# Performance work log

Hardware: AMD Instinct MI355X
Metric: run time of the kernel (lower is better)

Reference implementation:

```python
import jax, jax.numpy as jnp
import numpy as np

B, T, C, H = 2, 2048, 1024, 16
D = C // H  # head dim = 64
NEG_MIN = jnp.finfo(jnp.float32).min


def setup_inputs() -> dict:
    key = jax.random.key(0)
    ks = jax.random.split(key, 5)
    std = 0.02
    return {
        "x": jax.random.normal(ks[0], (B, T, C), dtype=jnp.float32),
        "Wq": std * jax.random.normal(ks[1], (C, C), dtype=jnp.float32),
        "bq": jnp.zeros((C,), dtype=jnp.float32),
        "Wk": std * jax.random.normal(ks[2], (C, C), dtype=jnp.float32),
        "bk": jnp.zeros((C,), dtype=jnp.float32),
        "Wv": std * jax.random.normal(ks[3], (C, C), dtype=jnp.float32),
        "bv": jnp.zeros((C,), dtype=jnp.float32),
        "Wo": (std / np.sqrt(24.0)) * jax.random.normal(ks[4], (C, C), dtype=jnp.float32),
        "bo": jnp.zeros((C,), dtype=jnp.float32),
    }


def reference(x, Wq, bq, Wk, bk, Wv, bv, Wo, bo):
    # QKV projections -> (B, H, T, D)
    def proj(W, b):
        return (x @ W + b).reshape(B, T, H, D).transpose(0, 2, 1, 3)

    q = proj(Wq, bq)
    k = proj(Wk, bk)
    v = proj(Wv, bv)

    # full scores (B, H, T, T), causal mask, softmax
    attn = jnp.einsum("bhqd,bhkd->bhqk", q, k) / jnp.sqrt(jnp.float32(D))
    mask = jnp.tril(jnp.ones((T, T), dtype=bool))[None, None]
    attn = jnp.where(mask, attn, NEG_MIN)
    scores = jax.nn.softmax(attn, axis=-1)

    out = jnp.einsum("bhqk,bhkd->bhqd", scores, v)
    out = out.transpose(0, 2, 1, 3).reshape(B, T, C)
    return out @ Wo + bo
```

## Files before the change

### kernel.cpp

```cpp
#include <hip/hip_runtime.h>
#include <stdint.h>
#include <stddef.h>


#define B_SZ 2
#define T_SZ 2048
#define C_SZ 1024
#define H_SZ 16
#define D_SZ 64
#define M_SZ (B_SZ * T_SZ)
#define BHTD (B_SZ * H_SZ * T_SZ * D_SZ)
#define CC (C_SZ * C_SZ)
#define SM_SHIFT 12.0f

typedef __attribute__((ext_vector_type(8))) __bf16 bf16x8;
typedef __attribute__((ext_vector_type(4))) float f32x4;
typedef __attribute__((ext_vector_type(16))) float f32x16;

__device__ __forceinline__ unsigned short f2bf(float f) {
    union { float f; unsigned u; } v; v.f = f;
    v.u += 0x7fffu + ((v.u >> 16) & 1u);
    return (unsigned short)(v.u >> 16);
}

__device__ __forceinline__ unsigned pkbf(float lo, float hi_) {
    union { unsigned u; __bf16 h[2]; } r;
    r.h[0] = (__bf16)lo; r.h[1] = (__bf16)hi_;
    return r.u;
}

__device__ __forceinline__ float fexp2(float x) {
    float r;
    asm volatile("v_exp_f32 %0, %1\n\ts_nop 0" : "=v"(r) : "v"(x));
    return r;
}

__device__ __forceinline__ void load_lds16(const unsigned short* g, unsigned short* l) {
    __builtin_amdgcn_global_load_lds(
        (const __attribute__((address_space(1))) void*)g,
        (__attribute__((address_space(3))) void*)l, 16, 0, 0);
}


__global__ void cvt_x_kernel(const float4* __restrict__ in, ushort4* __restrict__ out, int n4) {
    int stride = gridDim.x * blockDim.x;
    for (int i = blockIdx.x * blockDim.x + threadIdx.x; i < n4; i += stride) {
        float4 v = in[i];
        ushort4 o;
        o.x = f2bf(v.x); o.y = f2bf(v.y); o.z = f2bf(v.z); o.w = f2bf(v.w);
        out[i] = o;
    }
}

__global__ __launch_bounds__(256) void transpose_cvt_kernel(
    const float* __restrict__ W0, const float* __restrict__ W1,
    const float* __restrict__ W2, const float* __restrict__ W3,
    unsigned short* __restrict__ T0, unsigned short* __restrict__ T1,
    unsigned short* __restrict__ T2, unsigned short* __restrict__ T3)
{
    __shared__ float tile[32][33];
    const float* W; unsigned short* Wt;
    switch (blockIdx.z) {
        case 0: W = W0; Wt = T0; break;
        case 1: W = W1; Wt = T1; break;
        case 2: W = W2; Wt = T2; break;
        default: W = W3; Wt = T3; break;
    }
    const int tx = threadIdx.x, ty = threadIdx.y;
    const int n0 = blockIdx.x * 32, k0 = blockIdx.y * 32;
    #pragma unroll
    for (int i = 0; i < 4; i++)
        tile[ty + i * 8][tx] = W[(size_t)(k0 + ty + i * 8) * C_SZ + n0 + tx];
    __syncthreads();
    #pragma unroll
    for (int i = 0; i < 4; i++)
        Wt[(size_t)(n0 + ty + i * 8) * C_SZ + k0 + tx] = f2bf(tile[tx][ty + i * 8]);
}

__global__ __launch_bounds__(256) void vt_kernel(
    const unsigned short* __restrict__ V, unsigned short* __restrict__ Vt)
{
    __shared__ unsigned short tile[32][33];
    const int bh = blockIdx.z;
    const int t0 = blockIdx.x * 32, d0 = blockIdx.y * 32;
    const unsigned short* src = V + (size_t)bh * T_SZ * D_SZ;
    unsigned short* dst = Vt + (size_t)bh * T_SZ * D_SZ;
    const int tx = threadIdx.x, ty = threadIdx.y;
    #pragma unroll
    for (int i = 0; i < 4; i++)
        tile[ty + i * 8][tx] = src[(size_t)(t0 + ty + i * 8) * D_SZ + d0 + tx];
    __syncthreads();
    #pragma unroll
    for (int i = 0; i < 4; i++)
        dst[(size_t)(d0 + ty + i * 8) * T_SZ + t0 + tx] = tile[tx][ty + i * 8];
}


__device__ __forceinline__ void gemm_tile_core(
    const unsigned short* __restrict__ A,
    const unsigned short* __restrict__ Bt,
    unsigned short* As, unsigned short* Bs,
    int m0, int n0, f32x4 acc[4][4])
{
    const int tid = threadIdx.x;
    const int lane = tid & 63;
    const int w = tid >> 6;
    const int l15 = lane & 15, lg = lane >> 4;
    const int wr = (w >> 1) * 64, wc = (w & 1) * 64;

    const unsigned short* Ag0 = A + (size_t)(m0 + (tid >> 2)) * C_SZ + (tid & 3) * 8;
    const unsigned short* Ag1 = Ag0 + (size_t)64 * C_SZ;
    const unsigned short* Bg0 = Bt + (size_t)(n0 + (tid >> 2)) * C_SZ + (tid & 3) * 8;
    const unsigned short* Bg1 = Bg0 + (size_t)64 * C_SZ;
    unsigned short* As0 = As + w * 512;
    unsigned short* As1 = As + 2048 + w * 512;
    unsigned short* Bs0 = Bs + w * 512;
    unsigned short* Bs1 = Bs + 2048 + w * 512;

    for (int k0 = 0; k0 < C_SZ; k0 += 32) {
        load_lds16(Ag0 + k0, As0);
        load_lds16(Ag1 + k0, As1);
        load_lds16(Bg0 + k0, Bs0);
        load_lds16(Bg1 + k0, Bs1);
        __syncthreads();
        bf16x8 af[4], bfv[4];
        const bf16x8* Ap = (const bf16x8*)As;
        const bf16x8* Bp = (const bf16x8*)Bs;
        #pragma unroll
        for (int m = 0; m < 4; m++) af[m] = Ap[(wr + m * 16 + l15) * 4 + lg];
        #pragma unroll
        for (int n = 0; n < 4; n++) bfv[n] = Bp[(wc + n * 16 + l15) * 4 + lg];
        #pragma unroll
        for (int m = 0; m < 4; m++)
            #pragma unroll
            for (int n = 0; n < 4; n++)
                acc[m][n] = __builtin_amdgcn_mfma_f32_16x16x32_bf16(af[m], bfv[n], acc[m][n], 0, 0, 0);
        __syncthreads();
    }
}

__global__ __launch_bounds__(256) void gemm_qkv_kernel(
    const unsigned short* __restrict__ A,
    const unsigned short* __restrict__ WtBase,
    const float* __restrict__ bq, const float* __restrict__ bk, const float* __restrict__ bv,
    unsigned short* __restrict__ QKV, unsigned short* __restrict__ Vtmp)
{
    __shared__ unsigned short As[4096], Bs[4096];
    const int z = blockIdx.x >> 3;
    const unsigned short* Bt = WtBase + (size_t)z * CC;
    const float* bias = (z == 0) ? bq : (z == 1) ? bk : bv;
    const float scale = (z == 0) ? 0.18033688011112042f : 1.0f;
    unsigned short* Out = (z == 2) ? Vtmp : QKV + (size_t)z * BHTD;

    f32x4 acc[4][4];
    f32x4 zero4 = {0.f, 0.f, 0.f, 0.f};
    #pragma unroll
    for (int m = 0; m < 4; m++)
        #pragma unroll
        for (int n = 0; n < 4; n++) acc[m][n] = zero4;

    const int m0 = blockIdx.y * 128, n0 = (blockIdx.x & 7) * 128;
    gemm_tile_core(A, Bt, As, Bs, m0, n0, acc);

    const int lane = threadIdx.x & 63;
    const int w = threadIdx.x >> 6;
    const int l15 = lane & 15, lg = lane >> 4;
    const int wr = (w >> 1) * 64, wc = (w & 1) * 64;
    #pragma unroll
    for (int n = 0; n < 4; n++) {
        const int col = n0 + wc + n * 16 + l15;
        const float bias_v = bias[col];
        const int h = col >> 6, d = col & 63;
        #pragma unroll
        for (int m = 0; m < 4; m++) {
            #pragma unroll
            for (int j = 0; j < 4; j++) {
                const int row = m0 + wr + m * 16 + lg * 4 + j;
                const int b = row >> 11, t = row & (T_SZ - 1);
                Out[(((size_t)(b * H_SZ + h)) * T_SZ + t) * D_SZ + d] =
                    f2bf((acc[m][n][j] + bias_v) * scale);
            }
        }
    }
}

__global__ __launch_bounds__(256) void gemm_out_kernel(
    const unsigned short* __restrict__ A,
    const unsigned short* __restrict__ Bt,
    const float* __restrict__ bo,
    float* __restrict__ Out)
{
    __shared__ unsigned short As[2048], Bs[4096];
    const int tid = threadIdx.x;
    const int lane = tid & 63;
    const int w = tid >> 6;
    const int l15 = lane & 15, lg = lane >> 4;
    const int wc = w * 32;
    const int m0 = blockIdx.y * 64, n0 = blockIdx.x * 128;

    const unsigned short* Ag  = A + (size_t)(m0 + (tid >> 2)) * C_SZ + (tid & 3) * 8;
    const unsigned short* Bg0 = Bt + (size_t)(n0 + (tid >> 2)) * C_SZ + (tid & 3) * 8;
    const unsigned short* Bg1 = Bg0 + (size_t)64 * C_SZ;
    unsigned short* As0 = As + w * 512;
    unsigned short* Bs0 = Bs + w * 512;
    unsigned short* Bs1 = Bs + 2048 + w * 512;

    f32x4 acc[4][2];
    f32x4 zero4 = {0.f, 0.f, 0.f, 0.f};
    #pragma unroll
    for (int m = 0; m < 4; m++)
        #pragma unroll
        for (int n = 0; n < 2; n++) acc[m][n] = zero4;

    for (int k0 = 0; k0 < C_SZ; k0 += 32) {
        load_lds16(Ag + k0, As0);
        load_lds16(Bg0 + k0, Bs0);
        load_lds16(Bg1 + k0, Bs1);
        __syncthreads();
        bf16x8 af[4], bfv[2];
        const bf16x8* Ap = (const bf16x8*)As;
        const bf16x8* Bp = (const bf16x8*)Bs;
        #pragma unroll
        for (int m = 0; m < 4; m++) af[m] = Ap[(m * 16 + l15) * 4 + lg];
        #pragma unroll
        for (int n = 0; n < 2; n++) bfv[n] = Bp[(wc + n * 16 + l15) * 4 + lg];
        #pragma unroll
        for (int m = 0; m < 4; m++)
            #pragma unroll
            for (int n = 0; n < 2; n++)
                acc[m][n] = __builtin_amdgcn_mfma_f32_16x16x32_bf16(af[m], bfv[n], acc[m][n], 0, 0, 0);
        __syncthreads();
    }

    #pragma unroll
    for (int n = 0; n < 2; n++) {
        const int col = n0 + wc + n * 16 + l15;
        const float bias_v = bo[col];
        #pragma unroll
        for (int m = 0; m < 4; m++) {
            #pragma unroll
            for (int j = 0; j < 4; j++) {
                const int row = m0 + m * 16 + lg * 4 + j;
                Out[(size_t)row * C_SZ + col] = acc[m][n][j] + bias_v;
            }
        }
    }
}

__global__ __launch_bounds__(512) void attn_fwd_kernel(
    const unsigned short* __restrict__ Q,
    const unsigned short* __restrict__ K,
    const unsigned short* __restrict__ Vt,
    unsigned short* __restrict__ O)
{
    const int idx = blockIdx.x;
    const int qt = (idx < 256) ? (15 - (idx >> 5)) : ((idx - 256) >> 5);
    const int bh = idx & 31;
    const int w8 = threadIdx.x >> 6;
    const int grp = w8 >> 2;
    const int wg = w8 & 3;
    const int lane = threadIdx.x & 63;
    const int l31 = lane & 31, hi = lane >> 5;
    const int qw = qt * 128 + 32 * wg;

    const unsigned short* Qh = Q + (size_t)bh * T_SZ * D_SZ;
    const unsigned short* Kh = K + (size_t)bh * T_SZ * D_SZ;
    const unsigned short* Vh = Vt + (size_t)bh * T_SZ * D_SZ;

    __shared__ __align__(16) unsigned short smem[32768];

    const int c0 = wg * 64 + lane;
    const int row0 = c0 >> 3;
    const int sw0 = (c0 & 7) ^ (row0 & 7);
    const int koff0 = row0 * 64 + sw0 * 8;
    const int voff0 = row0 * T_SZ + sw0 * 8;
    const int ldsb0 = wg * 512;
    unsigned short* gbase = smem + grp * 16384;

    bf16x8 qf[4];
    #pragma unroll
    for (int j = 0; j < 4; j++)
        qf[j] = *(const bf16x8*)&Qh[(size_t)(qw + l31) * D_SZ + j * 16 + 8 * hi];

    f32x16 acc[2];
    #pragma unroll
    for (int r = 0; r < 16; r++) { acc[0][r] = 0.f; acc[1][r] = 0.f; }
    float lrun = 0.f;

    const int tlast = (qw + 31) >> 6;
    const int ntb = qt + 1;
    const int tg0 = grp * ntb;
    const int qrow = qw + l31;
    const int swl = l31 & 7;

    {
        const unsigned short* Kt = Kh + (size_t)tg0 * 64 * D_SZ;
        const unsigned short* Vtt = Vh + tg0 * 64;
        load_lds16(Kt + koff0, gbase + ldsb0);
        load_lds16(Kt + koff0 + 2048, gbase + 2048 + ldsb0);
        load_lds16(Vtt + voff0, gbase + 4096 + ldsb0);
        load_lds16(Vtt + voff0 + 32 * T_SZ, gbase + 6144 + ldsb0);
    }

    for (int tt = 0; tt < ntb; ++tt) {
        const int tg = tg0 + tt;
        if (tt + 1 < ntb) {
            unsigned short* Bd = gbase + ((tt + 1) & 1) * 8192;
            const unsigned short* Kt = Kh + (size_t)(tg + 1) * 64 * D_SZ;
            const unsigned short* Vtt = Vh + (tg + 1) * 64;
            load_lds16(Kt + koff0, Bd + ldsb0);
            load_lds16(Kt + koff0 + 2048, Bd + 2048 + ldsb0);
            load_lds16(Vtt + voff0, Bd + 4096 + ldsb0);
            load_lds16(Vtt + voff0 + 32 * T_SZ, Bd + 6144 + ldsb0);
            asm volatile("s_waitcnt vmcnt(4)" ::: "memory");
        } else {
            asm volatile("s_waitcnt vmcnt(0)" ::: "memory");
        }
        __builtin_amdgcn_s_barrier();

        if (tg <= tlast) {
            const unsigned short* Ks = gbase + (tt & 1) * 8192;
            const unsigned short* Vs = Ks + 4096;
            const int k0 = tg * 64;

            f32x16 s[2];
            __builtin_amdgcn_s_setprio(1);
            #pragma unroll
            for (int kb = 0; kb < 2; ++kb) {
                bf16x8 kf[4];
                #pragma unroll
                for (int j = 0; j < 4; ++j) {
                    const int ch = (j * 2 + hi) ^ swl;
                    kf[j] = *(const bf16x8*)&Ks[(kb * 32 + l31) * 64 + ch * 8];
                }
                f32x16 sc;
                #pragma unroll
                for (int r = 0; r < 16; r++) sc[r] = 0.f;
                #pragma unroll
                for (int j = 0; j < 4; ++j)
                    sc = __builtin_amdgcn_mfma_f32_32x32x16_bf16(kf[j], qf[j], sc, 0, 0, 0);
                s[kb] = sc;
            }
            __builtin_amdgcn_s_setprio(0);

            if (k0 + 63 > qw) {
                #pragma unroll
                for (int kb = 0; kb < 2; ++kb)
                    #pragma unroll
                    for (int r = 0; r < 16; ++r) {
                        const int kv = k0 + kb * 32 + (r & 3) + 8 * (r >> 2) + 4 * hi;
                        s[kb][r] = (kv > qrow) ? -3.0e38f : s[kb][r];
                    }
            }

            #pragma unroll
            for (int kb = 0; kb < 2; ++kb)
                #pragma unroll
                for (int r = 0; r < 16; r++) s[kb][r] = fexp2(s[kb][r] - SM_SHIFT);

            float ps0 = s[0][0] + s[1][0], ps1 = s[0][1] + s[1][1];
            float ps2 = s[0][2] + s[1][2], ps3 = s[0][3] + s[1][3];
            #pragma unroll
            for (int r = 4; r < 16; r += 4) {
                ps0 += s[0][r + 0] + s[1][r + 0];
                ps1 += s[0][r + 1] + s[1][r + 1];
                ps2 += s[0][r + 2] + s[1][r + 2];
                ps3 += s[0][r + 3] + s[1][r + 3];
            }
            float ps = (ps0 + ps1) + (ps2 + ps3);
            ps += __shfl_xor(ps, 32);
            lrun += ps;

            bf16x8 pf[2][2];
            #pragma unroll
            for (int kb = 0; kb < 2; ++kb) {
                #pragma unroll
                for (int ksl = 0; ksl < 2; ++ksl) {
                    unsigned a0 = pkbf(s[kb][8 * ksl + 0], s[kb][8 * ksl + 1]);
                    unsigned a1 = pkbf(s[kb][8 * ksl + 2], s[kb][8 * ksl + 3]);
                    unsigned b0 = pkbf(s[kb][8 * ksl + 4], s[kb][8 * ksl + 5]);
                    unsigned b1 = pkbf(s[kb][8 * ksl + 6], s[kb][8 * ksl + 7]);
                    asm volatile("v_permlane32_swap_b32 %0, %1" : "+v"(a0), "+v"(b0));
                    asm volatile("v_permlane32_swap_b32 %0, %1" : "+v"(a1), "+v"(b1));
                    union { unsigned u[4]; bf16x8 v; } fr;
                    fr.u[0] = a0; fr.u[1] = a1; fr.u[2] = b0; fr.u[3] = b1;
                    pf[kb][ksl] = fr.v;
                }
            }

            __builtin_amdgcn_s_setprio(1);
            #pragma unroll
            for (int dt = 0; dt < 2; ++dt)
                #pragma unroll
                for (int kb = 0; kb < 2; ++kb)
                    #pragma unroll
                    for (int ksl = 0; ksl < 2; ++ksl) {
                        const int ks = kb * 2 + ksl;
                        const int ch = (ks * 2 + hi) ^ swl;
                        const bf16x8 vf = *(const bf16x8*)&Vs[(dt * 32 + l31) * 64 + ch * 8];
                        acc[dt] = __builtin_amdgcn_mfma_f32_32x32x16_bf16(vf, pf[kb][ksl], acc[dt], 0, 0, 0);
                    }
            __builtin_amdgcn_s_setprio(0);
        }
        __builtin_amdgcn_s_barrier();
    }

    float* accf = (float*)smem;
    float* lsh = accf + 256 * 33;
    if (grp == 1) {
        const int li = wg * 64 + lane;
        #pragma unroll
        for (int r = 0; r < 16; r++) {
            accf[li * 33 + r] = acc[0][r];
            accf[li * 33 + 16 + r] = acc[1][r];
        }
        if (hi == 0) lsh[wg * 32 + l31] = lrun;
    }
    __builtin_amdgcn_s_barrier();
    if (grp == 0) {
        const int li = wg * 64 + lane;
        const float l1 = lsh[wg * 32 + l31];
        const float inv = 1.0f / (lrun + l1);
        #pragma unroll
        for (int r = 0; r < 16; r++) {
            acc[0][r] = (acc[0][r] + accf[li * 33 + r]) * inv;
            acc[1][r] = (acc[1][r] + accf[li * 33 + 16 + r]) * inv;
        }
    }
    __builtin_amdgcn_s_barrier();

    if (grp == 0) {
        unsigned short* ot = smem + wg * 2304;
        #pragma unroll
        for (int g = 0; g < 4; g++) {
            ushort4 wa, wb;
            wa.x = f2bf(acc[0][4 * g + 0]); wa.y = f2bf(acc[0][4 * g + 1]);
            wa.z = f2bf(acc[0][4 * g + 2]); wa.w = f2bf(acc[0][4 * g + 3]);
            wb.x = f2bf(acc[1][4 * g + 0]); wb.y = f2bf(acc[1][4 * g + 1]);
            wb.z = f2bf(acc[1][4 * g + 2]); wb.w = f2bf(acc[1][4 * g + 3]);
            *(ushort4*)&ot[l31 * 72 + 8 * g + 4 * hi] = wa;
            *(ushort4*)&ot[l31 * 72 + 32 + 8 * g + 4 * hi] = wb;
        }
        const int b = bh >> 4, h = bh & 15;
        #pragma unroll
        for (int pss = 0; pss < 4; pss++) {
            const int q = pss * 8 + (lane >> 3);
            const uint4 val = *(const uint4*)&ot[q * 72 + (lane & 7) * 8];
            *(uint4*)&O[((size_t)(b * T_SZ + qw + q)) * C_SZ + h * D_SZ + (lane & 7) * 8] = val;
        }
    }
}


extern "C" void kernel_launch(void* const* d_in, const int* in_sizes, int n_in,
                              void* d_out, int out_size, void* d_ws, size_t ws_size,
                              hipStream_t stream)
{
    const float* x  = (const float*)d_in[0];
    const float* Wq = (const float*)d_in[1];
    const float* bq = (const float*)d_in[2];
    const float* Wk = (const float*)d_in[3];
    const float* bk = (const float*)d_in[4];
    const float* Wv = (const float*)d_in[5];
    const float* bv = (const float*)d_in[6];
    const float* Wo = (const float*)d_in[7];
    const float* bo = (const float*)d_in[8];

    uint8_t* ws = (uint8_t*)d_ws;
    unsigned short* XB   = (unsigned short*)(ws);
    unsigned short* WT   = (unsigned short*)(ws + (8u  << 20));
    unsigned short* QKV  = (unsigned short*)(ws + (16u << 20));
    unsigned short* Vtmp = (unsigned short*)(ws + (40u << 20));

    cvt_x_kernel<<<2048, 256, 0, stream>>>((const float4*)x, (ushort4*)XB, M_SZ * C_SZ / 4);
    transpose_cvt_kernel<<<dim3(32, 32, 4), dim3(32, 8), 0, stream>>>(
        Wq, Wk, Wv, Wo, WT, WT + CC, WT + 2 * (size_t)CC, WT + 3 * (size_t)CC);
    gemm_qkv_kernel<<<dim3(24, 32), 256, 0, stream>>>(XB, WT, bq, bk, bv, QKV, Vtmp);
    vt_kernel<<<dim3(64, 2, 32), dim3(32, 8), 0, stream>>>(Vtmp, QKV + 2 * (size_t)BHTD);
    attn_fwd_kernel<<<512, 512, 0, stream>>>(
        QKV, QKV + BHTD, QKV + 2 * (size_t)BHTD, Vtmp);
    gemm_out_kernel<<<dim3(8, 64), 256, 0, stream>>>(Vtmp, WT + 3 * (size_t)CC, bo, (float*)d_out);
}
```

Baseline: 115.6 us.

## Halve attention tiles to 64-query blocks and 32-key tiles with 4-wave workgroups

Restructures the attention kernel so each workgroup handles 64 query rows with 4 waves (2 per key-split group) instead of 128 rows with 8 waves. K/V tiles shrink from 64 to 32 keys, the LDS swizzle for V changes to a 4-chunk pattern, and the grid doubles to 1024 blocks. The aim is finer causal granularity, less wasted masked work, more blocks for load balance, and lower LDS use per block for higher occupancy. In exchange it doubles the number of loop iterations and barriers per key range and halves K/V reuse per load.

```diff
diff --git a/kernel.cpp b/kernel.cpp
--- a/kernel.cpp
+++ b/kernel.cpp
@@ -247,35 +247,37 @@
     }
 }
 
-__global__ __launch_bounds__(512) void attn_fwd_kernel(
+__global__ __launch_bounds__(256) void attn_fwd_kernel(
     const unsigned short* __restrict__ Q,
     const unsigned short* __restrict__ K,
     const unsigned short* __restrict__ Vt,
     unsigned short* __restrict__ O)
 {
     const int idx = blockIdx.x;
-    const int qt = (idx < 256) ? (15 - (idx >> 5)) : ((idx - 256) >> 5);
+    const int qb = (idx < 512) ? (31 - (idx >> 5)) : ((idx - 512) >> 5);
     const int bh = idx & 31;
-    const int w8 = threadIdx.x >> 6;
-    const int grp = w8 >> 2;
-    const int wg = w8 & 3;
+    const int w4 = threadIdx.x >> 6;
+    const int grp = w4 >> 1;
+    const int wg = w4 & 1;
     const int lane = threadIdx.x & 63;
     const int l31 = lane & 31, hi = lane >> 5;
-    const int qw = qt * 128 + 32 * wg;
+    const int qw = qb * 64 + 32 * wg;
 
     const unsigned short* Qh = Q + (size_t)bh * T_SZ * D_SZ;
     const unsigned short* Kh = K + (size_t)bh * T_SZ * D_SZ;
     const unsigned short* Vh = Vt + (size_t)bh * T_SZ * D_SZ;
 
-    __shared__ __align__(16) unsigned short smem[32768];
+    __shared__ __align__(16) unsigned short smem[16384];
 
     const int c0 = wg * 64 + lane;
-    const int row0 = c0 >> 3;
-    const int sw0 = (c0 & 7) ^ (row0 & 7);
-    const int koff0 = row0 * 64 + sw0 * 8;
-    const int voff0 = row0 * T_SZ + sw0 * 8;
-    const int ldsb0 = wg * 512;
-    unsigned short* gbase = smem + grp * 16384;
+    const int krow0 = c0 >> 3;
+    const int ksw0 = (c0 & 7) ^ (krow0 & 7);
+    const int koff0 = krow0 * 64 + ksw0 * 8;
+    const int vrow0 = c0 >> 2;
+    const int vsw0 = (c0 & 3) ^ (vrow0 & 3);
+    const int voff0 = vrow0 * T_SZ + vsw0 * 8;
+    unsigned short* gbase = smem + grp * 8192;
+    const int wdst = wg * 512;
 
     bf16x8 qf[4];
     #pragma unroll
@@ -287,31 +289,31 @@
     for (int r = 0; r < 16; r++) { acc[0][r] = 0.f; acc[1][r] = 0.f; }
     float lrun = 0.f;
 
-    const int tlast = (qw + 31) >> 6;
-    const int ntb = qt + 1;
+    const int tlast = (qw + 31) >> 5;
+    const int ntb = qb + 1;
     const int tg0 = grp * ntb;
     const int qrow = qw + l31;
-    const int swl = l31 & 7;
+    const int swl7 = l31 & 7, swl3 = l31 & 3;
 
     {
-        const unsigned short* Kt = Kh + (size_t)tg0 * 64 * D_SZ;
-        const unsigned short* Vtt = Vh + tg0 * 64;
-        load_lds16(Kt + koff0, gbase + ldsb0);
-        load_lds16(Kt + koff0 + 2048, gbase + 2048 + ldsb0);
-        load_lds16(Vtt + voff0, gbase + 4096 + ldsb0);
-        load_lds16(Vtt + voff0 + 32 * T_SZ, gbase + 6144 + ldsb0);
+        const unsigned short* Kt = Kh + (size_t)tg0 * 32 * D_SZ;
+        const unsigned short* Vtt = Vh + tg0 * 32;
+        load_lds16(Kt + koff0, gbase + wdst);
+        load_lds16(Kt + koff0 + 1024, gbase + 1024 + wdst);
+        load_lds16(Vtt + voff0, gbase + 2048 + wdst);
+        load_lds16(Vtt + voff0 + 32 * T_SZ, gbase + 3072 + wdst);
     }
 
     for (int tt = 0; tt < ntb; ++tt) {
         const int tg = tg0 + tt;
         if (tt + 1 < ntb) {
-            unsigned short* Bd = gbase + ((tt + 1) & 1) * 8192;
-            const unsigned short* Kt = Kh + (size_t)(tg + 1) * 64 * D_SZ;
-            const unsigned short* Vtt = Vh + (tg + 1) * 64;
-            load_lds16(Kt + koff0, Bd + ldsb0);
-            load_lds16(Kt + koff0 + 2048, Bd + 2048 + ldsb0);
-            load_lds16(Vtt + voff0, Bd + 4096 + ldsb0);
-            load_lds16(Vtt + voff0 + 32 * T_SZ, Bd + 6144 + ldsb0);
+            unsigned short* Bd = gbase + ((tt + 1) & 1) * 4096;
+            const unsigned short* Kt = Kh + (size_t)(tg + 1) * 32 * D_SZ;
+            const unsigned short* Vtt = Vh + (tg + 1) * 32;
+            load_lds16(Kt + koff0, Bd + wdst);
+            load_lds16(Kt + koff0 + 1024, Bd + 1024 + wdst);
+            load_lds16(Vtt + voff0, Bd + 2048 + wdst);
+            load_lds16(Vtt + voff0 + 32 * T_SZ, Bd + 3072 + wdst);
             asm volatile("s_waitcnt vmcnt(4)" ::: "memory");
         } else {
             asm volatile("s_waitcnt vmcnt(0)" ::: "memory");
@@ -319,94 +321,76 @@
         __builtin_amdgcn_s_barrier();
 
         if (tg <= tlast) {
-            const unsigned short* Ks = gbase + (tt & 1) * 8192;
-            const unsigned short* Vs = Ks + 4096;
-            const int k0 = tg * 64;
-
-            f32x16 s[2];
+            const unsigned short* Ks = gbase + (tt & 1) * 4096;
+            const unsigned short* Vs = Ks + 2048;
+            const int k0 = tg * 32;
+
+            f32x16 s;
             __builtin_amdgcn_s_setprio(1);
-            #pragma unroll
-            for (int kb = 0; kb < 2; ++kb) {
+            {
                 bf16x8 kf[4];
                 #pragma unroll
                 for (int j = 0; j < 4; ++j) {
-                    const int ch = (j * 2 + hi) ^ swl;
-                    kf[j] = *(const bf16x8*)&Ks[(kb * 32 + l31) * 64 + ch * 8];
+                    const int ch = (j * 2 + hi) ^ swl7;
+                    kf[j] = *(const bf16x8*)&Ks[l31 * 64 + ch * 8];
                 }
-                f32x16 sc;
                 #pragma unroll
-                for (int r = 0; r < 16; r++) sc[r] = 0.f;
+                for (int r = 0; r < 16; r++) s[r] = 0.f;
                 #pragma unroll
                 for (int j = 0; j < 4; ++j)
-                    sc = __builtin_amdgcn_mfma_f32_32x32x16_bf16(kf[j], qf[j], sc, 0, 0, 0);
-                s[kb] = sc;
+                    s = __builtin_amdgcn_mfma_f32_32x32x16_bf16(kf[j], qf[j], s, 0, 0, 0);
             }
             __builtin_amdgcn_s_setprio(0);
 
-            if (k0 + 63 > qw) {
+            if (k0 + 31 > qw) {
                 #pragma unroll
-                for (int kb = 0; kb < 2; ++kb)
-                    #pragma unroll
-                    for (int r = 0; r < 16; ++r) {
-                        const int kv = k0 + kb * 32 + (r & 3) + 8 * (r >> 2) + 4 * hi;
-                        s[kb][r] = (kv > qrow) ? -3.0e38f : s[kb][r];
-                    }
+                for (int r = 0; r < 16; ++r) {
+                    const int kv = k0 + (r & 3) + 8 * (r >> 2) + 4 * hi;
+                    s[r] = (kv > qrow) ? -3.0e38f : s[r];
+                }
             }
 
             #pragma unroll
-            for (int kb = 0; kb < 2; ++kb)
-                #pragma unroll
-                for (int r = 0; r < 16; r++) s[kb][r] = fexp2(s[kb][r] - SM_SHIFT);
-
-            float ps0 = s[0][0] + s[1][0], ps1 = s[0][1] + s[1][1];
-            float ps2 = s[0][2] + s[1][2], ps3 = s[0][3] + s[1][3];
-            #pragma unroll
-            for (int r = 4; r < 16; r += 4) {
-                ps0 += s[0][r + 0] + s[1][r + 0];
-                ps1 += s[0][r + 1] + s[1][r + 1];
-                ps2 += s[0][r + 2] + s[1][r + 2];
-                ps3 += s[0][r + 3] + s[1][r + 3];
-            }
+            for (int r = 0; r < 16; r++) s[r] = fexp2(s[r] - SM_SHIFT);
+
+            float ps0 = s[0] + s[4], ps1 = s[1] + s[5];
+            float ps2 = s[2] + s[6], ps3 = s[3] + s[7];
+            ps0 += s[8] + s[12]; ps1 += s[9] + s[13];
+            ps2 += s[10] + s[14]; ps3 += s[11] + s[15];
             float ps = (ps0 + ps1) + (ps2 + ps3);
             ps += __shfl_xor(ps, 32);
             lrun += ps;
 
-            bf16x8 pf[2][2];
-            #pragma unroll
-            for (int kb = 0; kb < 2; ++kb) {
+            bf16x8 pf[2];
+            #pragma unroll
+            for (int ksl = 0; ksl < 2; ++ksl) {
+                unsigned a0 = pkbf(s[8 * ksl + 0], s[8 * ksl + 1]);
+                unsigned a1 = pkbf(s[8 * ksl + 2], s[8 * ksl + 3]);
+                unsigned b0 = pkbf(s[8 * ksl + 4], s[8 * ksl + 5]);
+                unsigned b1 = pkbf(s[8 * ksl + 6], s[8 * ksl + 7]);
+                asm volatile("v_permlane32_swap_b32 %0, %1" : "+v"(a0), "+v"(b0));
+                asm volatile("v_permlane32_swap_b32 %0, %1" : "+v"(a1), "+v"(b1));
+                union { unsigned u[4]; bf16x8 v; } fr;
+                fr.u[0] = a0; fr.u[1] = a1; fr.u[2] = b0; fr.u[3] = b1;
+                pf[ksl] = fr.v;
+            }
+
+            __builtin_amdgcn_s_setprio(1);
+            #pragma unroll
+            for (int dt = 0; dt < 2; ++dt)
                 #pragma unroll
                 for (int ksl = 0; ksl < 2; ++ksl) {
-                    unsigned a0 = pkbf(s[kb][8 * ksl + 0], s[kb][8 * ksl + 1]);
-                    unsigned a1 = pkbf(s[kb][8 * ksl + 2], s[kb][8 * ksl + 3]);
-                    unsigned b0 = pkbf(s[kb][8 * ksl + 4], s[kb][8 * ksl + 5]);
-                    unsigned b1 = pkbf(s[kb][8 * ksl + 6], s[kb][8 * ksl + 7]);
-                    asm volatile("v_permlane32_swap_b32 %0, %1" : "+v"(a0), "+v"(b0));
-                    asm volatile("v_permlane32_swap_b32 %0, %1" : "+v"(a1), "+v"(b1));
-                    union { unsigned u[4]; bf16x8 v; } fr;
-                    fr.u[0] = a0; fr.u[1] = a1; fr.u[2] = b0; fr.u[3] = b1;
-                    pf[kb][ksl] = fr.v;
+                    const int ch = (ksl * 2 + hi) ^ swl3;
+                    const bf16x8 vf = *(const bf16x8*)&Vs[(dt * 32 + l31) * 32 + ch * 8];
+                    acc[dt] = __builtin_amdgcn_mfma_f32_32x32x16_bf16(vf, pf[ksl], acc[dt], 0, 0, 0);
                 }
-            }
-
-            __builtin_amdgcn_s_setprio(1);
-            #pragma unroll
-            for (int dt = 0; dt < 2; ++dt)
-                #pragma unroll
-                for (int kb = 0; kb < 2; ++kb)
-                    #pragma unroll
-                    for (int ksl = 0; ksl < 2; ++ksl) {
-                        const int ks = kb * 2 + ksl;
-                        const int ch = (ks * 2 + hi) ^ swl;
-                        const bf16x8 vf = *(const bf16x8*)&Vs[(dt * 32 + l31) * 64 + ch * 8];
-                        acc[dt] = __builtin_amdgcn_mfma_f32_32x32x16_bf16(vf, pf[kb][ksl], acc[dt], 0, 0, 0);
-                    }
             __builtin_amdgcn_s_setprio(0);
         }
         __builtin_amdgcn_s_barrier();
     }
 
     float* accf = (float*)smem;
-    float* lsh = accf + 256 * 33;
+    float* lsh = accf + 128 * 33;
     if (grp == 1) {
         const int li = wg * 64 + lane;
         #pragma unroll
@@ -477,7 +461,7 @@
         Wq, Wk, Wv, Wo, WT, WT + CC, WT + 2 * (size_t)CC, WT + 3 * (size_t)CC);
     gemm_qkv_kernel<<<dim3(24, 32), 256, 0, stream>>>(XB, WT, bq, bk, bv, QKV, Vtmp);
     vt_kernel<<<dim3(64, 2, 32), dim3(32, 8), 0, stream>>>(Vtmp, QKV + 2 * (size_t)BHTD);
-    attn_fwd_kernel<<<512, 512, 0, stream>>>(
+    attn_fwd_kernel<<<1024, 256, 0, stream>>>(
         QKV, QKV + BHTD, QKV + 2 * (size_t)BHTD, Vtmp);
     gemm_out_kernel<<<dim3(8, 64), 256, 0, stream>>>(Vtmp, WT + 3 * (size_t)CC, bo, (float*)d_out);
 }
```

After: 116.3 us. About the same (+0.6%).

## Widen GEMM K-step to 64 with XOR-swizzled LDS and fuse prep kernels

Applied to the files above, without the earlier changes.

The shared GEMM tile core now loads 64-wide K slices per iteration into LDS using an XOR swizzle on 16-byte chunks, halving the barrier count and avoiding LDS bank conflicts on fragment reads. The x conversion and weight transpose kernels are merged into one launch using an extra grid z-slice. The larger LDS footprint may reduce occupancy, and any caller with smaller shared buffers would overflow.

```diff
diff --git a/kernel.cpp b/kernel.cpp
--- a/kernel.cpp
+++ b/kernel.cpp
@@ -42,25 +42,31 @@
 }
 
 
-__global__ void cvt_x_kernel(const float4* __restrict__ in, ushort4* __restrict__ out, int n4) {
-    int stride = gridDim.x * blockDim.x;
-    for (int i = blockIdx.x * blockDim.x + threadIdx.x; i < n4; i += stride) {
-        float4 v = in[i];
-        ushort4 o;
-        o.x = f2bf(v.x); o.y = f2bf(v.y); o.z = f2bf(v.z); o.w = f2bf(v.w);
-        out[i] = o;
-    }
-}
-
-__global__ __launch_bounds__(256) void transpose_cvt_kernel(
+__global__ __launch_bounds__(256) void prep_kernel(
+    const float* __restrict__ x,
     const float* __restrict__ W0, const float* __restrict__ W1,
     const float* __restrict__ W2, const float* __restrict__ W3,
+    ushort4* __restrict__ XB,
     unsigned short* __restrict__ T0, unsigned short* __restrict__ T1,
     unsigned short* __restrict__ T2, unsigned short* __restrict__ T3)
 {
+    const int z = blockIdx.z;
+    if (z == 4) {
+        const float4* in = (const float4*)x;
+        const int tid = (blockIdx.y * 32 + blockIdx.x) * 256 + threadIdx.y * 32 + threadIdx.x;
+        #pragma unroll
+        for (int k = 0; k < 4; k++) {
+            const int i = tid + k * 262144;
+            float4 v = in[i];
+            ushort4 o;
+            o.x = f2bf(v.x); o.y = f2bf(v.y); o.z = f2bf(v.z); o.w = f2bf(v.w);
+            XB[i] = o;
+        }
+        return;
+    }
     __shared__ float tile[32][33];
     const float* W; unsigned short* Wt;
-    switch (blockIdx.z) {
+    switch (z) {
         case 0: W = W0; Wt = T0; break;
         case 1: W = W1; Wt = T1; break;
         case 2: W = W2; Wt = T2; break;
@@ -95,7 +101,6 @@
         dst[(size_t)(d0 + ty + i * 8) * T_SZ + t0 + tx] = tile[tx][ty + i * 8];
 }
 
-
 __device__ __forceinline__ void gemm_tile_core(
     const unsigned short* __restrict__ A,
     const unsigned short* __restrict__ Bt,
@@ -108,33 +113,38 @@
     const int l15 = lane & 15, lg = lane >> 4;
     const int wr = (w >> 1) * 64, wc = (w & 1) * 64;
 
-    const unsigned short* Ag0 = A + (size_t)(m0 + (tid >> 2)) * C_SZ + (tid & 3) * 8;
-    const unsigned short* Ag1 = Ag0 + (size_t)64 * C_SZ;
-    const unsigned short* Bg0 = Bt + (size_t)(n0 + (tid >> 2)) * C_SZ + (tid & 3) * 8;
-    const unsigned short* Bg1 = Bg0 + (size_t)64 * C_SZ;
-    unsigned short* As0 = As + w * 512;
-    unsigned short* As1 = As + 2048 + w * 512;
-    unsigned short* Bs0 = Bs + w * 512;
-    unsigned short* Bs1 = Bs + 2048 + w * 512;
-
-    for (int k0 = 0; k0 < C_SZ; k0 += 32) {
-        load_lds16(Ag0 + k0, As0);
-        load_lds16(Ag1 + k0, As1);
-        load_lds16(Bg0 + k0, Bs0);
-        load_lds16(Bg1 + k0, Bs1);
+    const int rA = lane >> 3;
+    const int sA = ((lane & 7) ^ rA) * 8;
+    const unsigned short* Ab = A + ((size_t)m0 + w * 8 + rA) * C_SZ + sA;
+    const unsigned short* Bb = Bt + ((size_t)n0 + w * 8 + rA) * C_SZ + sA;
+    unsigned short* AsW = As + w * 512;
+    unsigned short* BsW = Bs + w * 512;
+    const int sw = l15 & 7;
+
+    for (int k0 = 0; k0 < C_SZ; k0 += 64) {
+        #pragma unroll
+        for (int ii = 0; ii < 4; ii++)
+            load_lds16(Ab + (size_t)(ii * 32) * C_SZ + k0, AsW + ii * 2048);
+        #pragma unroll
+        for (int ii = 0; ii < 4; ii++)
+            load_lds16(Bb + (size_t)(ii * 32) * C_SZ + k0, BsW + ii * 2048);
         __syncthreads();
-        bf16x8 af[4], bfv[4];
-        const bf16x8* Ap = (const bf16x8*)As;
-        const bf16x8* Bp = (const bf16x8*)Bs;
-        #pragma unroll
-        for (int m = 0; m < 4; m++) af[m] = Ap[(wr + m * 16 + l15) * 4 + lg];
-        #pragma unroll
-        for (int n = 0; n < 4; n++) bfv[n] = Bp[(wc + n * 16 + l15) * 4 + lg];
-        #pragma unroll
-        for (int m = 0; m < 4; m++)
+        #pragma unroll
+        for (int kk = 0; kk < 2; kk++) {
+            bf16x8 af[4], bfv[4];
+            const int ch = ((kk * 4 + lg) ^ sw) * 8;
+            #pragma unroll
+            for (int m = 0; m < 4; m++)
+                af[m] = *(const bf16x8*)&As[(wr + m * 16 + l15) * 64 + ch];
             #pragma unroll
             for (int n = 0; n < 4; n++)
-                acc[m][n] = __builtin_amdgcn_mfma_f32_16x16x32_bf16(af[m], bfv[n], acc[m][n], 0, 0, 0);
+                bfv[n] = *(const bf16x8*)&Bs[(wc + n * 16 + l15) * 64 + ch];
+            #pragma unroll
+            for (int m = 0; m < 4; m++)
+                #pragma unroll
+                for (int n = 0; n < 4; n++)
+                    acc[m][n] = __builtin_amdgcn_mfma_f32_16x16x32_bf16(af[m], bfv[n], acc[m][n], 0, 0, 0);
+        }
         __syncthreads();
     }
 }
@@ -145,7 +155,7 @@
     const float* __restrict__ bq, const float* __restrict__ bk, const float* __restrict__ bv,
     unsigned short* __restrict__ QKV, unsigned short* __restrict__ Vtmp)
 {
-    __shared__ unsigned short As[4096], Bs[4096];
+    __shared__ __align__(16) unsigned short As[8192], Bs[8192];
     const int z = blockIdx.x >> 3;
     const unsigned short* Bt = WtBase + (size_t)z * CC;
     const float* bias = (z == 0) ? bq : (z == 1) ? bk : bv;
@@ -472,9 +482,9 @@
     unsigned short* QKV  = (unsigned short*)(ws + (16u << 20));
     unsigned short* Vtmp = (unsigned short*)(ws + (40u << 20));
 
-    cvt_x_kernel<<<2048, 256, 0, stream>>>((const float4*)x, (ushort4*)XB, M_SZ * C_SZ / 4);
-    transpose_cvt_kernel<<<dim3(32, 32, 4), dim3(32, 8), 0, stream>>>(
-        Wq, Wk, Wv, Wo, WT, WT + CC, WT + 2 * (size_t)CC, WT + 3 * (size_t)CC);
+    prep_kernel<<<dim3(32, 32, 5), dim3(32, 8), 0, stream>>>(
+        x, Wq, Wk, Wv, Wo, (ushort4*)XB,
+        WT, WT + CC, WT + 2 * (size_t)CC, WT + 3 * (size_t)CC);
     gemm_qkv_kernel<<<dim3(24, 32), 256, 0, stream>>>(XB, WT, bq, bk, bv, QKV, Vtmp);
     vt_kernel<<<dim3(64, 2, 32), dim3(32, 8), 0, stream>>>(Vtmp, QKV + 2 * (size_t)BHTD);
     attn_fwd_kernel<<<512, 512, 0, stream>>>(
```

After: 117.9 us. No clear change (+2.0%).
